# Kernel tuning notes

Hardware: AMD Instinct MI355X
Metric: run time of the kernel (lower is better)

Reference implementation:

```python
import jax, jax.numpy as jnp
import numpy as np


def setup_inputs() -> dict:
    key = jax.random.key(0)
    k1, k2, k3 = jax.random.split(key, 3)
    M, P, K = 4096, 64, 128
    color_seqs = jax.random.normal(k1, (M, P, K), dtype=jnp.float32)
    mew = jax.random.normal(k2, (M, K), dtype=jnp.float32)
    sigma = jax.random.normal(k3, (M, K, K), dtype=jnp.float32)
    return {"color_seqs": color_seqs, "mew": mew, "sigma": sigma}


def reference(color_seqs, mew, sigma):
    # shifted: (m, p, k)
    shifted = color_seqs - mew[:, None, :]
    # scores[m,p] = - (c-mu) Sigma (c-mu)^T  (negated batched quadratic form)
    scores = -jnp.einsum('mpk,mkl,mpl->mp', shifted, sigma, shifted)
    # softmax over the context (p) dimension, matching nn.Softmax(dim=1)
    return jax.nn.softmax(scores, axis=1)
```

## Files before the change

kernel.cpp:

```cpp
#include <hip/hip_runtime.h>

#define SROW 132

typedef _Float16 half8 __attribute__((ext_vector_type(8)));
typedef float f32x4 __attribute__((ext_vector_type(4)));


__global__ __launch_bounds__(256, 3)
void quadform_softmax(const float* __restrict__ color,
                      const float* __restrict__ mew,
                      const float* __restrict__ sigma,
                      float* __restrict__ out) {
  __shared__ __align__(16) float s_all[4 * 16 * SROW];
  __shared__ __align__(16) _Float16 Bp[2][8][64][8];
  __shared__ float scores_lds[64];

  const int tid  = threadIdx.x;
  const int wv   = tid >> 6;
  const int lane = tid & 63;
  const int m    = blockIdx.x;

  float* sw = &s_all[wv * (16 * SROW)];
  const float* sg  = sigma + (size_t)m * 16384;
  const float* sgh = sg + wv * (8 * 128);

  float p0,p1,p2,p3,p4,p5,p6,p7,p8,p9,p10,p11,p12,p13,p14,p15;

#define SIG_LOAD(CH) do {                                               \
    const float* gp = sgh + (CH) * (32 * 128);                          \
    p0  = gp[0*128 + lane];       p1  = gp[1*128 + lane];               \
    p2  = gp[2*128 + lane];       p3  = gp[3*128 + lane];               \
    p4  = gp[4*128 + lane];       p5  = gp[5*128 + lane];               \
    p6  = gp[6*128 + lane];       p7  = gp[7*128 + lane];               \
    p8  = gp[0*128 + 64 + lane];  p9  = gp[1*128 + 64 + lane];          \
    p10 = gp[2*128 + 64 + lane];  p11 = gp[3*128 + 64 + lane];          \
    p12 = gp[4*128 + 64 + lane];  p13 = gp[5*128 + 64 + lane];          \
    p14 = gp[6*128 + 64 + lane];  p15 = gp[7*128 + 64 + lane];          \
  } while (0)

#define CV(H, L, I, X) do { _Float16 t_ = (_Float16)(X);                \
    H[I] = t_; L[I] = (_Float16)((X) - (float)t_); } while (0)

#define SIG_WRITE() do {                                                \
    half8 hi0, lo0, hi1, lo1;                                           \
    CV(hi0, lo0, 0, p0);  CV(hi0, lo0, 1, p1);                          \
    CV(hi0, lo0, 2, p2);  CV(hi0, lo0, 3, p3);                          \
    CV(hi0, lo0, 4, p4);  CV(hi0, lo0, 5, p5);                          \
    CV(hi0, lo0, 6, p6);  CV(hi0, lo0, 7, p7);                          \
    CV(hi1, lo1, 0, p8);  CV(hi1, lo1, 1, p9);                          \
    CV(hi1, lo1, 2, p10); CV(hi1, lo1, 3, p11);                         \
    CV(hi1, lo1, 4, p12); CV(hi1, lo1, 5, p13);                         \
    CV(hi1, lo1, 6, p14); CV(hi1, lo1, 7, p15);                         \
    const int t0_ = lane >> 4, slot_ = wv * 16 + (lane & 15);           \
    *reinterpret_cast<half8*>(&Bp[0][t0_    ][slot_][0]) = hi0;         \
    *reinterpret_cast<half8*>(&Bp[1][t0_    ][slot_][0]) = lo0;         \
    *reinterpret_cast<half8*>(&Bp[0][t0_ + 4][slot_][0]) = hi1;         \
    *reinterpret_cast<half8*>(&Bp[1][t0_ + 4][slot_][0]) = lo1;         \
  } while (0)

  SIG_LOAD(0);

  {
    const int hh = lane >> 5;
    const int q  = lane & 31;
    const float4* c4 = reinterpret_cast<const float4*>(color + (size_t)m * 8192)
                       + (size_t)(16 * wv) * 32;
    const float4 mw = reinterpret_cast<const float4*>(mew + (size_t)m * 128)[q];
#pragma unroll
    for (int r = 0; r < 8; ++r) {
      const int row = hh + 2 * r;
      float4 v = c4[row * 32 + q];
      v.x -= mw.x; v.y -= mw.y; v.z -= mw.z; v.w -= mw.w;
      *reinterpret_cast<float4*>(&sw[row * SROW + 4 * q]) = v;
    }
  }

  const int hl = lane >> 4;
  const int rl = lane & 15;
  half8 aH0, aL0, aH1, aL1, aH2, aL2, aH3, aL3;

#define A_BUILD(Q, AH, AL) do {                                         \
    const float* sa_ = &sw[rl * SROW + (Q) * 32 + 8 * hl];              \
    float4 x0_ = *reinterpret_cast<const float4*>(sa_);                 \
    float4 x1_ = *reinterpret_cast<const float4*>(sa_ + 4);             \
    CV(AH, AL, 0, x0_.x); CV(AH, AL, 1, x0_.y);                         \
    CV(AH, AL, 2, x0_.z); CV(AH, AL, 3, x0_.w);                         \
    CV(AH, AL, 4, x1_.x); CV(AH, AL, 5, x1_.y);                         \
    CV(AH, AL, 6, x1_.z); CV(AH, AL, 7, x1_.w);                         \
  } while (0)

  A_BUILD(0, aH0, aL0);
  A_BUILD(1, aH1, aL1);
  A_BUILD(2, aH2, aL2);
  A_BUILD(3, aH3, aL3);

  SIG_WRITE();
  __syncthreads();

  f32x4 acc[8];
#pragma unroll
  for (int t = 0; t < 8; ++t) acc[t] = (f32x4){0.f, 0.f, 0.f, 0.f};

#define MT(T, AH, AL) do {                                                    \
    half8 bh_ = *reinterpret_cast<const half8*>(&Bp[0][T][lane][0]);          \
    half8 bl_ = *reinterpret_cast<const half8*>(&Bp[1][T][lane][0]);          \
    acc[T] = __builtin_amdgcn_mfma_f32_16x16x32_f16(AH, bh_, acc[T], 0,0,0);  \
    acc[T] = __builtin_amdgcn_mfma_f32_16x16x32_f16(AH, bl_, acc[T], 0,0,0);  \
    acc[T] = __builtin_amdgcn_mfma_f32_16x16x32_f16(AL, bh_, acc[T], 0,0,0);  \
  } while (0)

#define MFMA_CHUNK(AH, AL) do {                                         \
    MT(0, AH, AL); MT(1, AH, AL); MT(2, AH, AL); MT(3, AH, AL);         \
    MT(4, AH, AL); MT(5, AH, AL); MT(6, AH, AL); MT(7, AH, AL);         \
  } while (0)

  SIG_LOAD(1);
  MFMA_CHUNK(aH0, aL0);
  __syncthreads();
  SIG_WRITE();
  __syncthreads();

  SIG_LOAD(2);
  MFMA_CHUNK(aH1, aL1);
  __syncthreads();
  SIG_WRITE();
  __syncthreads();

  SIG_LOAD(3);
  MFMA_CHUNK(aH2, aL2);
  __syncthreads();
  SIG_WRITE();
  __syncthreads();

  MFMA_CHUNK(aH3, aL3);

  float part[4] = {0.f, 0.f, 0.f, 0.f};
#pragma unroll
  for (int t = 0; t < 8; ++t) {
#pragma unroll
    for (int r = 0; r < 4; ++r) {
      float sv = sw[(4 * hl + r) * SROW + 16 * t + rl];
      part[r] = fmaf(acc[t][r], sv, part[r]);
    }
  }
#pragma unroll
  for (int r = 0; r < 4; ++r) {
    part[r] += __shfl_xor(part[r], 1, 64);
    part[r] += __shfl_xor(part[r], 2, 64);
    part[r] += __shfl_xor(part[r], 4, 64);
    part[r] += __shfl_xor(part[r], 8, 64);
  }
  if (rl == 0) {
#pragma unroll
    for (int r = 0; r < 4; ++r)
      scores_lds[wv * 16 + 4 * hl + r] = -part[r];
  }
  __syncthreads();

  if (tid < 64) {
    float sc = scores_lds[tid];
    float mx = sc;
#pragma unroll
    for (int off = 1; off < 64; off <<= 1) mx = fmaxf(mx, __shfl_xor(mx, off, 64));
    float e = __expf(sc - mx);
    float s = e;
#pragma unroll
    for (int off = 1; off < 64; off <<= 1) s += __shfl_xor(s, off, 64);
    out[(size_t)m * 64 + tid] = e / s;
  }
}

extern "C" void kernel_launch(void* const* d_in, const int* in_sizes, int n_in,
                              void* d_out, int out_size, void* d_ws, size_t ws_size,
                              hipStream_t stream) {
  const float* color = (const float*)d_in[0];
  const float* mew   = (const float*)d_in[1];
  const float* sigma = (const float*)d_in[2];
  float* out = (float*)d_out;
  const int M = in_sizes[1] / 128;
  quadform_softmax<<<M, 256, 0, stream>>>(color, mew, sigma, out);
}
```

Baseline: 431.9 us.

## Load sigma rows directly into MFMA A operands, drop LDS staging and barriers

Sigma is now read with float4 loads straight into registers, split into hi/lo fp16 halves and used as the A operand, while the shifted colour rows in LDS become the B operand. This removes the fp16 Bp LDS buffer and the sync/write/sync round trips per chunk, with sigma loads double-buffered in registers. Each wave now covers 32 sigma rows against all 64 positions and writes per-wave partial scores that are summed before the softmax. The trade-off is more LDS reads of the colour data per chunk and higher register pressure from the prefetch buffers.

Result: no change. 435.1 us (+0.7%).

```diff
diff --git a/kernel.cpp b/kernel.cpp
--- a/kernel.cpp
+++ b/kernel.cpp
@@ -12,53 +12,29 @@
                       const float* __restrict__ sigma,
                       float* __restrict__ out) {
   __shared__ __align__(16) float s_all[4 * 16 * SROW];
-  __shared__ __align__(16) _Float16 Bp[2][8][64][8];
-  __shared__ float scores_lds[64];
+  __shared__ float scores_part[4][64];
 
   const int tid  = threadIdx.x;
   const int wv   = tid >> 6;
   const int lane = tid & 63;
+  const int hl   = lane >> 4;
+  const int rl   = lane & 15;
   const int m    = blockIdx.x;
 
   float* sw = &s_all[wv * (16 * SROW)];
-  const float* sg  = sigma + (size_t)m * 16384;
-  const float* sgh = sg + wv * (8 * 128);
+  const float4* sig4 = reinterpret_cast<const float4*>(sigma + (size_t)m * 16384);
 
-  float p0,p1,p2,p3,p4,p5,p6,p7,p8,p9,p10,p11,p12,p13,p14,p15;
+  const int arow0 = 32 * wv + rl;
 
-#define SIG_LOAD(CH) do {                                               \
-    const float* gp = sgh + (CH) * (32 * 128);                          \
-    p0  = gp[0*128 + lane];       p1  = gp[1*128 + lane];               \
-    p2  = gp[2*128 + lane];       p3  = gp[3*128 + lane];               \
-    p4  = gp[4*128 + lane];       p5  = gp[5*128 + lane];               \
-    p6  = gp[6*128 + lane];       p7  = gp[7*128 + lane];               \
-    p8  = gp[0*128 + 64 + lane];  p9  = gp[1*128 + 64 + lane];          \
-    p10 = gp[2*128 + 64 + lane];  p11 = gp[3*128 + 64 + lane];          \
-    p12 = gp[4*128 + 64 + lane];  p13 = gp[5*128 + 64 + lane];          \
-    p14 = gp[6*128 + 64 + lane];  p15 = gp[7*128 + 64 + lane];          \
+#define SIG_ISSUE(Q, PA, PB, PC, PD) do {                         \
+    PA = sig4[(arow0)      * 32 + 8 * (Q) + 2 * hl];              \
+    PB = sig4[(arow0)      * 32 + 8 * (Q) + 2 * hl + 1];          \
+    PC = sig4[(arow0 + 16) * 32 + 8 * (Q) + 2 * hl];              \
+    PD = sig4[(arow0 + 16) * 32 + 8 * (Q) + 2 * hl + 1];          \
   } while (0)
 
-#define CV(H, L, I, X) do { _Float16 t_ = (_Float16)(X);                \
-    H[I] = t_; L[I] = (_Float16)((X) - (float)t_); } while (0)
-
-#define SIG_WRITE() do {                                                \
-    half8 hi0, lo0, hi1, lo1;                                           \
-    CV(hi0, lo0, 0, p0);  CV(hi0, lo0, 1, p1);                          \
-    CV(hi0, lo0, 2, p2);  CV(hi0, lo0, 3, p3);                          \
-    CV(hi0, lo0, 4, p4);  CV(hi0, lo0, 5, p5);                          \
-    CV(hi0, lo0, 6, p6);  CV(hi0, lo0, 7, p7);                          \
-    CV(hi1, lo1, 0, p8);  CV(hi1, lo1, 1, p9);                          \
-    CV(hi1, lo1, 2, p10); CV(hi1, lo1, 3, p11);                         \
-    CV(hi1, lo1, 4, p12); CV(hi1, lo1, 5, p13);                         \
-    CV(hi1, lo1, 6, p14); CV(hi1, lo1, 7, p15);                         \
-    const int t0_ = lane >> 4, slot_ = wv * 16 + (lane & 15);           \
-    *reinterpret_cast<half8*>(&Bp[0][t0_    ][slot_][0]) = hi0;         \
-    *reinterpret_cast<half8*>(&Bp[1][t0_    ][slot_][0]) = lo0;         \
-    *reinterpret_cast<half8*>(&Bp[0][t0_ + 4][slot_][0]) = hi1;         \
-    *reinterpret_cast<half8*>(&Bp[1][t0_ + 4][slot_][0]) = lo1;         \
-  } while (0)
-
-  SIG_LOAD(0);
+  float4 P00, P01, P10, P11, N00, N01, N10, N11;
+  SIG_ISSUE(0, P00, P01, P10, P11);
 
   {
     const int hh = lane >> 5;
@@ -74,91 +50,81 @@
       *reinterpret_cast<float4*>(&sw[row * SROW + 4 * q]) = v;
     }
   }
+  __syncthreads();
 
-  const int hl = lane >> 4;
-  const int rl = lane & 15;
-  half8 aH0, aL0, aH1, aL1, aH2, aL2, aH3, aL3;
+#define CV(H, L, I, X) do { _Float16 t_ = (_Float16)(X);          \
+    H[I] = t_; L[I] = (_Float16)((X) - (float)t_); } while (0)
 
-#define A_BUILD(Q, AH, AL) do {                                         \
-    const float* sa_ = &sw[rl * SROW + (Q) * 32 + 8 * hl];              \
-    float4 x0_ = *reinterpret_cast<const float4*>(sa_);                 \
-    float4 x1_ = *reinterpret_cast<const float4*>(sa_ + 4);             \
-    CV(AH, AL, 0, x0_.x); CV(AH, AL, 1, x0_.y);                         \
-    CV(AH, AL, 2, x0_.z); CV(AH, AL, 3, x0_.w);                         \
-    CV(AH, AL, 4, x1_.x); CV(AH, AL, 5, x1_.y);                         \
-    CV(AH, AL, 6, x1_.z); CV(AH, AL, 7, x1_.w);                         \
+#define B_BUILD(Q, N, BH, BL) do {                                        \
+    const float* sb_ = &s_all[(N) * (16 * SROW) + rl * SROW               \
+                              + 32 * (Q) + 8 * hl];                       \
+    float4 b0_ = *reinterpret_cast<const float4*>(sb_);                   \
+    float4 b1_ = *reinterpret_cast<const float4*>(sb_ + 4);               \
+    CV(BH, BL, 0, b0_.x); CV(BH, BL, 1, b0_.y);                           \
+    CV(BH, BL, 2, b0_.z); CV(BH, BL, 3, b0_.w);                           \
+    CV(BH, BL, 4, b1_.x); CV(BH, BL, 5, b1_.y);                           \
+    CV(BH, BL, 6, b1_.z); CV(BH, BL, 7, b1_.w);                           \
   } while (0)
 
-  A_BUILD(0, aH0, aL0);
-  A_BUILD(1, aH1, aL1);
-  A_BUILD(2, aH2, aL2);
-  A_BUILD(3, aH3, aL3);
-
-  SIG_WRITE();
-  __syncthreads();
+#define A_CONV(F0, F1, AH, AL) do {                                       \
+    CV(AH, AL, 0, (F0).x); CV(AH, AL, 1, (F0).y);                         \
+    CV(AH, AL, 2, (F0).z); CV(AH, AL, 3, (F0).w);                         \
+    CV(AH, AL, 4, (F1).x); CV(AH, AL, 5, (F1).y);                         \
+    CV(AH, AL, 6, (F1).z); CV(AH, AL, 7, (F1).w);                         \
+  } while (0)
 
   f32x4 acc[8];
 #pragma unroll
   for (int t = 0; t < 8; ++t) acc[t] = (f32x4){0.f, 0.f, 0.f, 0.f};
 
-#define MT(T, AH, AL) do {                                                    \
-    half8 bh_ = *reinterpret_cast<const half8*>(&Bp[0][T][lane][0]);          \
-    half8 bl_ = *reinterpret_cast<const half8*>(&Bp[1][T][lane][0]);          \
-    acc[T] = __builtin_amdgcn_mfma_f32_16x16x32_f16(AH, bh_, acc[T], 0,0,0);  \
-    acc[T] = __builtin_amdgcn_mfma_f32_16x16x32_f16(AH, bl_, acc[T], 0,0,0);  \
-    acc[T] = __builtin_amdgcn_mfma_f32_16x16x32_f16(AL, bh_, acc[T], 0,0,0);  \
+#define MT3(I, AH, AL, BH, BL) do {                                             \
+    acc[I] = __builtin_amdgcn_mfma_f32_16x16x32_f16(AH, BH, acc[I], 0, 0, 0);   \
+    acc[I] = __builtin_amdgcn_mfma_f32_16x16x32_f16(AL, BH, acc[I], 0, 0, 0);   \
+    acc[I] = __builtin_amdgcn_mfma_f32_16x16x32_f16(AH, BL, acc[I], 0, 0, 0);   \
   } while (0)
 
-#define MFMA_CHUNK(AH, AL) do {                                         \
-    MT(0, AH, AL); MT(1, AH, AL); MT(2, AH, AL); MT(3, AH, AL);         \
-    MT(4, AH, AL); MT(5, AH, AL); MT(6, AH, AL); MT(7, AH, AL);         \
-  } while (0)
+#define CHUNK(Q, PA, PB, PC, PD, QN, NA, NB, NC, ND, DO_PRE)          \
+  {                                                                   \
+    if (DO_PRE) { SIG_ISSUE(QN, NA, NB, NC, ND); }                    \
+    half8 bh0, bl0, bh1, bl1, bh2, bl2, bh3, bl3;                     \
+    B_BUILD(Q, 0, bh0, bl0); B_BUILD(Q, 1, bh1, bl1);                 \
+    B_BUILD(Q, 2, bh2, bl2); B_BUILD(Q, 3, bh3, bl3);                 \
+    half8 ah0, al0, ah1, al1;                                         \
+    A_CONV(PA, PB, ah0, al0); A_CONV(PC, PD, ah1, al1);               \
+    MT3(0, ah0, al0, bh0, bl0); MT3(1, ah0, al0, bh1, bl1);           \
+    MT3(2, ah0, al0, bh2, bl2); MT3(3, ah0, al0, bh3, bl3);           \
+    MT3(4, ah1, al1, bh0, bl0); MT3(5, ah1, al1, bh1, bl1);           \
+    MT3(6, ah1, al1, bh2, bl2); MT3(7, ah1, al1, bh3, bl3);           \
+  }
 
-  SIG_LOAD(1);
-  MFMA_CHUNK(aH0, aL0);
-  __syncthreads();
-  SIG_WRITE();
-  __syncthreads();
+  CHUNK(0, P00, P01, P10, P11, 1, N00, N01, N10, N11, 1)
+  CHUNK(1, N00, N01, N10, N11, 2, P00, P01, P10, P11, 1)
+  CHUNK(2, P00, P01, P10, P11, 3, N00, N01, N10, N11, 1)
+  CHUNK(3, N00, N01, N10, N11, 0, P00, P01, P10, P11, 0)
 
-  SIG_LOAD(2);
-  MFMA_CHUNK(aH1, aL1);
-  __syncthreads();
-  SIG_WRITE();
-  __syncthreads();
+#define DOT4(A, S) ((A)[0]*(S).x + (A)[1]*(S).y + (A)[2]*(S).z + (A)[3]*(S).w)
 
-  SIG_LOAD(3);
-  MFMA_CHUNK(aH2, aL2);
-  __syncthreads();
-  SIG_WRITE();
-  __syncthreads();
-
-  MFMA_CHUNK(aH3, aL3);
-
-  float part[4] = {0.f, 0.f, 0.f, 0.f};
+  float part[4];
 #pragma unroll
-  for (int t = 0; t < 8; ++t) {
-#pragma unroll
-    for (int r = 0; r < 4; ++r) {
-      float sv = sw[(4 * hl + r) * SROW + 16 * t + rl];
-      part[r] = fmaf(acc[t][r], sv, part[r]);
-    }
+  for (int n = 0; n < 4; ++n) {
+    const float* se = &s_all[n * (16 * SROW) + rl * SROW + 32 * wv + 4 * hl];
+    float4 s0 = *reinterpret_cast<const float4*>(se);
+    float4 s1 = *reinterpret_cast<const float4*>(se + 16);
+    part[n] = DOT4(acc[n], s0) + DOT4(acc[4 + n], s1);
   }
 #pragma unroll
-  for (int r = 0; r < 4; ++r) {
-    part[r] += __shfl_xor(part[r], 1, 64);
-    part[r] += __shfl_xor(part[r], 2, 64);
-    part[r] += __shfl_xor(part[r], 4, 64);
-    part[r] += __shfl_xor(part[r], 8, 64);
+  for (int n = 0; n < 4; ++n) {
+    part[n] += __shfl_xor(part[n], 16, 64);
+    part[n] += __shfl_xor(part[n], 32, 64);
   }
-  if (rl == 0) {
-#pragma unroll
-    for (int r = 0; r < 4; ++r)
-      scores_lds[wv * 16 + 4 * hl + r] = -part[r];
-  }
+  float myp = (hl == 0) ? part[0] : (hl == 1) ? part[1]
+            : (hl == 2) ? part[2] : part[3];
+  scores_part[wv][lane] = myp;
   __syncthreads();
 
   if (tid < 64) {
-    float sc = scores_lds[tid];
+    float sc = -(scores_part[0][tid] + scores_part[1][tid]
+               + scores_part[2][tid] + scores_part[3][tid]);
     float mx = sc;
 #pragma unroll
     for (int off = 1; off < 64; off <<= 1) mx = fmaxf(mx, __shfl_xor(mx, off, 64));
```
